# Performance work log

Measured on AMD Instinct MI355X. Metric: run time of the kernel, lower is better.

Reference implementation:

```python
import jax, jax.numpy as jnp
import numpy as np

N_ROI = 1024
N_CLASS = 21      # num_classes + 1
APP_DIM = 1024
D_F = 128
N_REL = 16
DIM_K = 64
DIM_G = 64


def loc2bbox(src, loc):
    # src, loc: [M,4] with (y0,x0,y1,x1) / (dy,dx,dh,dw)
    h = src[:, 2] - src[:, 0]
    w = src[:, 3] - src[:, 1]
    cy = src[:, 0] + 0.5 * h
    cx = src[:, 1] + 0.5 * w
    ncy = loc[:, 0] * h + cy
    ncx = loc[:, 1] * w + cx
    nh = jnp.exp(loc[:, 2]) * h
    nw = jnp.exp(loc[:, 3]) * w
    return jnp.stack([ncy - 0.5 * nh, ncx - 0.5 * nw,
                      ncy + 0.5 * nh, ncx + 0.5 * nw], axis=1)


def rank_embedding(n, feat_dim, wave_len=1000.0):
    rank = jnp.arange(n, dtype=jnp.float32)[:, None]
    fr = jnp.arange(feat_dim // 2, dtype=jnp.float32)
    dim_mat = 1.0 / (wave_len ** (fr / (feat_dim / 2.0)))
    mul = rank * dim_mat[None, :]
    return jnp.concatenate([jnp.sin(mul), jnp.cos(mul)], axis=-1)  # [n, feat_dim]


def positional_embedding(f_g, dim_g, wave_len=1000.0):
    # f_g: [N,4]; replicates the repo's PositionalEmbedding exactly
    x_min, y_min, x_max, y_max = jnp.split(f_g, 4, axis=1)  # [N,1] each
    cx = (x_min + x_max) * 0.5
    cy = (y_min + y_max) * 0.5
    w = (x_max - x_min) + 1.0
    h = (y_max - y_min) + 1.0
    dx = jnp.log(jnp.maximum(jnp.abs((cx - cx.T) / w), 1e-3))
    dy = jnp.log(jnp.maximum(jnp.abs((cy - cy.T) / h), 1e-3))
    dw = jnp.log(w / w.T)
    dh = jnp.log(h / h.T)
    pos = jnp.stack([dx, dy, dw, dh], axis=-1)               # [N,N,4]
    fr = jnp.arange(dim_g // 8, dtype=jnp.float32)
    dim_mat = 1.0 / (wave_len ** (fr / (dim_g / 8.0)))       # [dim_g/8]
    mul = (100.0 * pos)[..., None] * dim_mat                 # [N,N,4,dim_g/8]
    mul = mul.reshape(pos.shape[0], pos.shape[1], -1)
    return jnp.concatenate([jnp.sin(mul), jnp.cos(mul)], axis=-1)  # [N,N,dim_g]


def setup_inputs():
    key = jax.random.key(0)
    ks = jax.random.split(key, 16)
    yx = jax.random.uniform(ks[0], (N_ROI, 2), minval=0.0, maxval=500.0)
    hw = jax.random.uniform(ks[1], (N_ROI, 2), minval=16.0, maxval=128.0)
    sample_roi = jnp.concatenate([yx, yx + hw], axis=1)      # valid (y0,x0,y1,x1)
    roi_cls_loc = jax.random.normal(ks[2], (N_ROI, N_CLASS * 4)) * 0.5
    roi_score = jax.random.normal(ks[3], (N_ROI, N_CLASS))
    # force no background argmax -> nonzero() filter keeps all N (static shapes)
    roi_score = roi_score.at[:, 0].add(-10.0)
    appearance_features = jax.random.normal(ks[4], (N_ROI, APP_DIM))
    size = jnp.array([600, 800], dtype=jnp.int32)
    s = 0.02
    rank_w = jax.random.normal(ks[5], (APP_DIM, D_F)) * s
    rank_b = jnp.zeros((D_F,), jnp.float32)
    feat_w = jax.random.normal(ks[6], (APP_DIM, D_F)) * s
    feat_b = jnp.zeros((D_F,), jnp.float32)
    logit_w = jax.random.normal(ks[7], (APP_DIM, 1)) * s
    logit_b = jnp.zeros((1,), jnp.float32)
    wg_w = jax.random.normal(ks[8], (N_REL, DIM_G)) * s
    wg_b = jnp.full((N_REL,), 0.1, jnp.float32)  # keep some geo weights > 0
    wk_w = jax.random.normal(ks[9], (N_REL, D_F, DIM_K)) * s
    wk_b = jnp.zeros((N_REL, DIM_K), jnp.float32)
    wq_w = jax.random.normal(ks[10], (N_REL, D_F, DIM_K)) * s
    wq_b = jnp.zeros((N_REL, DIM_K), jnp.float32)
    wv_w = jax.random.normal(ks[11], (N_REL, D_F, DIM_K)) * s
    wv_b = jnp.zeros((N_REL, DIM_K), jnp.float32)
    return {"sample_roi": sample_roi, "roi_cls_loc": roi_cls_loc,
            "roi_score": roi_score, "appearance_features": appearance_features,
            "size": size,
            "rank_w": rank_w, "rank_b": rank_b, "feat_w": feat_w, "feat_b": feat_b,
            "logit_w": logit_w, "logit_b": logit_b,
            "wg_w": wg_w, "wg_b": wg_b, "wk_w": wk_w, "wk_b": wk_b,
            "wq_w": wq_w, "wq_b": wq_b, "wv_w": wv_w, "wv_b": wv_b}


def reference(sample_roi, roi_cls_loc, roi_score, appearance_features, size,
              rank_w, rank_b, feat_w, feat_b, logit_w, logit_b,
              wg_w, wg_b, wk_w, wk_b, wq_w, wq_b, wv_w, wv_b):
    n = sample_roi.shape[0]
    size_f = size.astype(jnp.float32)
    # loc denormalization (mean = 0)
    std = jnp.tile(jnp.array([0.1, 0.1, 0.2, 0.2], jnp.float32), N_CLASS)
    loc = (roi_cls_loc * std).reshape(-1, 4)                  # [N*21,4]
    roi_rep = jnp.broadcast_to(sample_roi[:, None, :], (n, N_CLASS, 4)).reshape(-1, 4)
    cls_bbox = loc2bbox(roi_rep, loc).reshape(n, N_CLASS, 4)
    # replicates original's clamp on class-strided slices of the [N,21,4] view
    cls_bbox = cls_bbox.at[:, 0::2].set(jnp.clip(cls_bbox[:, 0::2], 0.0, size_f[0]))
    cls_bbox = cls_bbox.at[:, 1::2].set(jnp.clip(cls_bbox[:, 1::2], 0.0, size_f[1]))
    prob_all = jax.nn.softmax(roi_score, axis=1)
    prob = jnp.max(prob_all, axis=-1)
    prob_argmax = jnp.argmax(prob_all, axis=-1)
    cls_bbox = cls_bbox[jnp.arange(n), prob_argmax]           # [N,4]
    # background filter; inputs guarantee all foreground -> static size n
    nz = jnp.nonzero(prob_argmax, size=n, fill_value=0)[0]
    prob_argmax = prob_argmax[nz]
    prob = prob[nz]
    cls_bbox = cls_bbox[nz]
    feats = appearance_features[nz]
    order = jnp.argsort(-prob)                                # descending
    sorted_prob = prob[order]
    sorted_cls_bboxes = cls_bbox[order]
    sorted_labels = prob_argmax[order]
    sorted_features = feats[order]
    nms_rank = rank_embedding(n, APP_DIM) @ rank_w + rank_b   # [N,D_F]
    emb_feat = sorted_features @ feat_w + feat_b + nms_rank   # [N,D_F]
    pos_emb = positional_embedding(sorted_cls_bboxes, DIM_G)  # [N,N,DIM_G]
    # 16 independent RelationUnits, batched as heads h
    w_g = jax.nn.relu(jnp.einsum('mng,hg->hmn', pos_emb, wg_w) + wg_b[:, None, None])
    k = jnp.einsum('nd,hdk->hnk', emb_feat, wk_w) + wk_b[:, None, :]
    q = jnp.einsum('nd,hdk->hnk', emb_feat, wq_w) + wq_b[:, None, :]
    v = jnp.einsum('nd,hdk->hnk', emb_feat, wv_w) + wv_b[:, None, :]
    # scaled_dot[m,n] = k_m . q_n (row m is 'key', softmax over n) per original
    scores = jnp.einsum('hmk,hnk->hmn', k, q) / np.sqrt(DIM_K).astype(np.float32)
    w_mn = jax.nn.softmax(jnp.log(jnp.maximum(w_g, 1e-6)) + scores, axis=-1)
    rel = jnp.einsum('hmn,hnk->hmk', w_mn, v)                 # [H,N,K]
    rel = rel.transpose(1, 0, 2).reshape(n, N_REL * DIM_K) + sorted_features
    s1 = jax.nn.sigmoid(rel @ logit_w + logit_b).reshape(-1)
    nms_scores = s1 * sorted_prob
    return nms_scores, sorted_labels - 1, sorted_cls_bboxes
```

## Files before the change

### kernel.cpp

```cpp
#include <hip/hip_runtime.h>
#include <hip/hip_bf16.h>
#include <math.h>

typedef unsigned long long u64;
typedef unsigned int u32;
typedef __hip_bfloat16 bf16;

#define N 1024
#define NCLS 21
#define APP 1024
#define DF 128
#define NH 16
#define DK 64

typedef __attribute__((ext_vector_type(8))) short short8v;
typedef __attribute__((ext_vector_type(4))) float float4v;
union U4S8 { uint4 u; short8v s; };

__device__ __forceinline__ float b2f(bf16 x) { return __bfloat162float(x); }
__device__ __forceinline__ ushort f2bu(float x) { bf16 b = __float2bfloat16(x); return *(ushort*)&b; }

__global__ void k_prep(const float* __restrict__ roi, const float* __restrict__ cls_loc,
                       const float* __restrict__ score, const int* __restrict__ size,
                       float* __restrict__ prob, int* __restrict__ label,
                       float* __restrict__ bbox, u64* __restrict__ keys)
{
    int i = blockIdx.x * 256 + threadIdx.x;
    if (i >= N) return;
    float s[NCLS];
    float mx = -1e30f; int am = 0;
    for (int c = 0; c < NCLS; c++) {
        s[c] = score[i * NCLS + c];
        if (s[c] > mx) { mx = s[c]; am = c; }
    }
    float sum = 0.f;
    for (int c = 0; c < NCLS; c++) sum += expf(s[c] - mx);
    float p = 1.0f / sum;

    float y0 = roi[i*4+0], x0 = roi[i*4+1];
    float y1 = roi[i*4+2], x1 = roi[i*4+3];
    float hh = y1 - y0, ww = x1 - x0;
    float cy = y0 + 0.5f * hh, cx = x0 + 0.5f * ww;
    float l0 = cls_loc[i*84 + am*4 + 0] * 0.1f;
    float l1 = cls_loc[i*84 + am*4 + 1] * 0.1f;
    float l2 = cls_loc[i*84 + am*4 + 2] * 0.2f;
    float l3 = cls_loc[i*84 + am*4 + 3] * 0.2f;
    float ncy = l0 * hh + cy, ncx = l1 * ww + cx;
    float nh = expf(l2) * hh, nw = expf(l3) * ww;
    float b0 = ncy - 0.5f * nh, b1 = ncx - 0.5f * nw;
    float b2v = ncy + 0.5f * nh, b3 = ncx + 0.5f * nw;
    float lim = ((am & 1) == 0) ? (float)size[0] : (float)size[1];
    b0  = fminf(fmaxf(b0, 0.f), lim);
    b1  = fminf(fmaxf(b1, 0.f), lim);
    b2v = fminf(fmaxf(b2v, 0.f), lim);
    b3  = fminf(fmaxf(b3, 0.f), lim);
    prob[i] = p; label[i] = am;
    bbox[i*4+0] = b0; bbox[i*4+1] = b1; bbox[i*4+2] = b2v; bbox[i*4+3] = b3;
    keys[i] = ((u64)(0xFFFFFFFFu - __float_as_uint(p)) << 32) | (u32)i;
}

__global__ void __launch_bounds__(256) k_rank(
        const u64* __restrict__ keys, const float* __restrict__ prob,
        const int* __restrict__ label, const float* __restrict__ bbox,
        int* __restrict__ order, float* __restrict__ sprob,
        float* __restrict__ sbbox, float* __restrict__ out)
{
    __shared__ u64 sk[N];
    int t = threadIdx.x;
    int i = blockIdx.x * 256 + t;
    for (int j = t; j < N; j += 256) sk[j] = keys[j];
    __syncthreads();
    u64 my = sk[i];
    int r = 0;
    for (int j = 0; j < N; j++) r += (sk[j] < my) ? 1 : 0;
    order[r] = i;
    sprob[r] = prob[i];
    float b0 = bbox[i*4+0], b1 = bbox[i*4+1], b2 = bbox[i*4+2], b3 = bbox[i*4+3];
    sbbox[r*4+0] = b0; sbbox[r*4+1] = b1; sbbox[r*4+2] = b2; sbbox[r*4+3] = b3;
    out[N + r] = (float)(label[i] - 1);
    out[2*N + r*4 + 0] = b0;
    out[2*N + r*4 + 1] = b1;
    out[2*N + r*4 + 2] = b2;
    out[2*N + r*4 + 3] = b3;
}

__global__ void __launch_bounds__(256) k_emb2(
        const int* __restrict__ order, const float* __restrict__ app,
        const float* __restrict__ feat_w, const float* __restrict__ rank_w,
        float* __restrict__ part)
{
    __shared__ ushort sA[64][72];
    __shared__ ushort sW[128][72];
    __shared__ int sOrd[64];
    int rt = blockIdx.x, dc = blockIdx.y, t = threadIdx.x;
    int r0 = rt * 64, d0 = dc * 64;
    int w = t >> 6, l = t & 63, l15 = l & 15, quad = l >> 4;
    if (t < 64) sOrd[t] = order[r0 + t];
    __syncthreads();

    float4v acc[8];
    #pragma unroll
    for (int nb = 0; nb < 8; nb++) acc[nb] = (float4v){0.f, 0.f, 0.f, 0.f};

    for (int phase = 0; phase < 2; phase++) {
        const float* Wsrc = phase ? rank_w : feat_w;
        #pragma unroll
        for (int it = 0; it < 32; it++) {
            int idx = t + it * 256;
            int d = idx >> 7, c = idx & 127;
            sW[c][d] = f2bu(Wsrc[(size_t)(d0 + d) * 128 + c]);
        }
        if (phase == 0) {
            #pragma unroll
            for (int it = 0; it < 16; it++) {
                int idx = t + it * 256;
                int r = idx >> 6, d = idx & 63;
                sA[r][d] = f2bu(app[(size_t)sOrd[r] * 1024 + d0 + d]);
            }
        } else {
            #pragma unroll
            for (int it = 0; it < 16; it++) {
                int idx = t + it * 256;
                int r = idx >> 6, d = idx & 63;
                int dgl = d0 + d;
                float irow = (float)(r0 + r);
                float val;
                if (dgl < 512) val = __sinf(irow * exp2f(-(float)dgl * 0.019464422f));
                else           val = __cosf(irow * exp2f(-(float)(dgl - 512) * 0.019464422f));
                sA[r][d] = f2bu(val);
            }
        }
        __syncthreads();
        U4S8 Af0, Af1;
        Af0.u = *(uint4*)&sA[w*16 + l15][quad*8];
        Af1.u = *(uint4*)&sA[w*16 + l15][32 + quad*8];
        #pragma unroll
        for (int nb = 0; nb < 8; nb++) {
            U4S8 Bf0, Bf1;
            Bf0.u = *(uint4*)&sW[nb*16 + l15][quad*8];
            Bf1.u = *(uint4*)&sW[nb*16 + l15][32 + quad*8];
            acc[nb] = __builtin_amdgcn_mfma_f32_16x16x32_bf16(Af0.s, Bf0.s, acc[nb], 0, 0, 0);
            acc[nb] = __builtin_amdgcn_mfma_f32_16x16x32_bf16(Af1.s, Bf1.s, acc[nb], 0, 0, 0);
        }
        __syncthreads();
    }
    #pragma unroll
    for (int reg = 0; reg < 4; reg++) {
        int row = r0 + w*16 + quad*4 + reg;
        #pragma unroll
        for (int nb = 0; nb < 8; nb++)
            part[((size_t)dc * 1024 + row) * 128 + nb*16 + l15] = acc[nb][reg];
    }
}

__global__ void k_embsum(const float* __restrict__ part,
                         const float* __restrict__ feat_b, const float* __restrict__ rank_b,
                         bf16* __restrict__ embb)
{
    int gid = blockIdx.x * 256 + threadIdx.x;
    int c = gid & 127;
    float acc = feat_b[c] + rank_b[c];
    for (int dc = 0; dc < 16; dc++) acc += part[(size_t)dc * 131072 + gid];
    embb[gid] = __float2bfloat16(acc);
}

__global__ void __launch_bounds__(256) k_qkv2(
        const bf16* __restrict__ embb,
        const float* __restrict__ wq, const float* __restrict__ bq,
        const float* __restrict__ wk, const float* __restrict__ bk,
        const float* __restrict__ wv, const float* __restrict__ bv,
        bf16* __restrict__ q, bf16* __restrict__ k, bf16* __restrict__ v)
{
    __shared__ ushort sWt[64][136];
    int t = threadIdx.x;
    int rt = blockIdx.x, h = blockIdx.y, mat = blockIdx.z;
    const float* W  = (mat == 0) ? wq : (mat == 1) ? wk : wv;
    const float* Bb = (mat == 0) ? bq : (mat == 1) ? bk : bv;
    bf16* Out       = (mat == 0) ? q  : (mat == 1) ? k  : v;

    #pragma unroll
    for (int i = 0; i < 32; i++) {
        int idx = t + i * 256;
        int d = idx >> 6, kk = idx & 63;
        sWt[kk][d] = f2bu(W[((size_t)h * 128 + d) * 64 + kk]);
    }
    int w = t >> 6, l = t & 63, l15 = l & 15, quad = l >> 4;
    float biasv[4];
    #pragma unroll
    for (int nb = 0; nb < 4; nb++) biasv[nb] = Bb[h * 64 + nb*16 + l15];
    __syncthreads();

    U4S8 Bf[4][4];
    #pragma unroll
    for (int nb = 0; nb < 4; nb++)
        #pragma unroll
        for (int kc = 0; kc < 4; kc++)
            Bf[nb][kc].u = *(uint4*)&sWt[nb*16 + l15][kc*32 + quad*8];

    const uint4* A4 = (const uint4*)embb;
    int r0 = rt * 256 + w * 64;
    ushort* outu = (ushort*)Out;
    for (int mb = 0; mb < 4; mb++) {
        int arow = r0 + mb*16 + l15;
        U4S8 Af[4];
        #pragma unroll
        for (int kc = 0; kc < 4; kc++) Af[kc].u = A4[(size_t)arow * 16 + kc*4 + quad];
        float4v acc[4];
        #pragma unroll
        for (int nb = 0; nb < 4; nb++) acc[nb] = (float4v){0.f, 0.f, 0.f, 0.f};
        #pragma unroll
        for (int kc = 0; kc < 4; kc++)
            #pragma unroll
            for (int nb = 0; nb < 4; nb++)
                acc[nb] = __builtin_amdgcn_mfma_f32_16x16x32_bf16(Af[kc].s, Bf[nb][kc].s, acc[nb], 0, 0, 0);
        #pragma unroll
        for (int reg = 0; reg < 4; reg++) {
            int orow = r0 + mb*16 + quad*4 + reg;
            #pragma unroll
            for (int nb = 0; nb < 4; nb++)
                outu[((size_t)h * N + orow) * 64 + nb*16 + l15] = f2bu(acc[nb][reg] + biasv[nb]);
        }
    }
}

__global__ void __launch_bounds__(256) k_geo2(
        const float* __restrict__ sbbox, const float* __restrict__ wgw,
        const float* __restrict__ wgb, bf16* __restrict__ lw)
{
    __shared__ ushort sE[256][72];
    __shared__ uint   sOut[NH][132];
    __shared__ float  mbb[4];
    int m = blockIdx.x, nc = blockIdx.y, t = threadIdx.x;
    int w = t >> 6, l = t & 63, l15 = l & 15, quad = l >> 4;

    if (t == 0) {
        float b0 = sbbox[m*4+0], b1 = sbbox[m*4+1], b2 = sbbox[m*4+2], b3 = sbbox[m*4+3];
        mbb[0] = (b0 + b2) * 0.5f; mbb[1] = (b1 + b3) * 0.5f;
        mbb[2] = b2 - b0 + 1.0f;   mbb[3] = b3 - b1 + 1.0f;
    }
    U4S8 Bg0, Bg1;
    #pragma unroll
    for (int j = 0; j < 8; j++) {
        ((ushort*)&Bg0)[j] = f2bu(wgw[l15*64 + quad*8 + j]);
        ((ushort*)&Bg1)[j] = f2bu(wgw[l15*64 + 32 + quad*8 + j]);
    }
    float bias = wgb[l15];
    __syncthreads();

    int n = nc * 256 + t;
    float b0 = sbbox[n*4+0], b1 = sbbox[n*4+1], b2 = sbbox[n*4+2], b3 = sbbox[n*4+3];
    float cxn = (b0 + b2) * 0.5f, cyn = (b1 + b3) * 0.5f;
    float wn = b2 - b0 + 1.0f, hn = b3 - b1 + 1.0f;
    float dx = __logf(fmaxf(fabsf((mbb[0] - cxn) / mbb[2]), 1e-3f));
    float dy = __logf(fmaxf(fabsf((mbb[1] - cyn) / mbb[3]), 1e-3f));
    float dw = __logf(mbb[2] / wn);
    float dh = __logf(mbb[3] / hn);
    float pos[4] = { dx, dy, dw, dh };
    const float dmt[8] = { 1.0f, 0.42169650342f, 0.177827941f, 0.0749894209f,
                           0.0316227766f, 0.01333521432f, 0.00562341325f, 0.00237137371f };
    float args[32];
    #pragma unroll
    for (int c = 0; c < 4; c++)
        #pragma unroll
        for (int f = 0; f < 8; f++) args[c*8 + f] = 100.0f * pos[c] * dmt[f];
    uint* rowp = (uint*)&sE[t][0];
    #pragma unroll
    for (int jj = 0; jj < 16; jj++) {
        float s0 = __sinf(args[2*jj]), s1 = __sinf(args[2*jj+1]);
        rowp[jj] = (uint)f2bu(s0) | ((uint)f2bu(s1) << 16);
    }
    #pragma unroll
    for (int jj = 0; jj < 16; jj++) {
        float c0 = __cosf(args[2*jj]), c1 = __cosf(args[2*jj+1]);
        rowp[16 + jj] = (uint)f2bu(c0) | ((uint)f2bu(c1) << 16);
    }
    __syncthreads();

    #pragma unroll
    for (int mt2 = 0; mt2 < 4; mt2++) {
        int prow = w*64 + mt2*16 + l15;
        U4S8 Af0, Af1;
        Af0.u = *(uint4*)&sE[prow][quad*8];
        Af1.u = *(uint4*)&sE[prow][32 + quad*8];
        float4v c = (float4v){0.f, 0.f, 0.f, 0.f};
        c = __builtin_amdgcn_mfma_f32_16x16x32_bf16(Af0.s, Bg0.s, c, 0, 0, 0);
        c = __builtin_amdgcn_mfma_f32_16x16x32_bf16(Af1.s, Bg1.s, c, 0, 0, 0);
        float v0 = __logf(fmaxf(fmaxf(c[0] + bias, 0.f), 1e-6f));
        float v1 = __logf(fmaxf(fmaxf(c[1] + bias, 0.f), 1e-6f));
        float v2 = __logf(fmaxf(fmaxf(c[2] + bias, 0.f), 1e-6f));
        float v3 = __logf(fmaxf(fmaxf(c[3] + bias, 0.f), 1e-6f));
        int pb = (w*64 + mt2*16 + quad*4) >> 1;
        sOut[l15][pb]     = (uint)f2bu(v0) | ((uint)f2bu(v1) << 16);
        sOut[l15][pb + 1] = (uint)f2bu(v2) | ((uint)f2bu(v3) << 16);
    }
    __syncthreads();
    uint* lwu = (uint*)lw;
    #pragma unroll
    for (int it = 0; it < 8; it++) {
        int idx = t + it * 256;
        int hh = idx >> 7, col = idx & 127;
        lwu[((size_t)hh << 19) + ((size_t)m << 9) + nc*128 + col] = sOut[hh][col];
    }
}

__global__ void __launch_bounds__(256) k_attn3(
        const bf16* __restrict__ q, const bf16* __restrict__ kmat,
        const bf16* __restrict__ v, const bf16* __restrict__ lw,
        bf16* __restrict__ rel)
{
    __shared__ uint sQu[64][36];
    __shared__ uint sVtu[64][36];
    __shared__ uint slwu[64][36];
    __shared__ uint sPu[4][16][36];

    int t = threadIdx.x;
    int mt = blockIdx.x, h = blockIdx.y;
    int m0 = mt * 64;
    int w = t >> 6, l = t & 63, l15 = l & 15, quad = l >> 4;

    U4S8 kf0, kf1;
    {
        const uint4* k4 = (const uint4*)kmat;
        size_t krow = ((size_t)h * N + m0 + w*16 + l15) * 8;
        kf0.u = k4[krow + quad];
        kf1.u = k4[krow + 4 + quad];
    }

    float4v O[4];
    float M[4], Z[4];
    #pragma unroll
    for (int i = 0; i < 4; i++) {
        O[i] = (float4v){0.f, 0.f, 0.f, 0.f};
        M[i] = -1e30f; Z[i] = 0.f;
    }

    const uint* qsrc = (const uint*)q;
    const uint* vsrc = (const uint*)v;
    const uint* lwsrc = (const uint*)lw;

    for (int tile = 0; tile < 16; tile++) {
        int n0 = tile * 64;
        #pragma unroll
        for (int i = 0; i < 8; i++) {
            int idx = t + i * 256;
            int nj = idx >> 5, kp = idx & 31;
            sQu[nj][kp] = qsrc[((size_t)h * N + n0 + nj) * 32 + kp];
        }
        #pragma unroll
        for (int i = 0; i < 4; i++) {
            int idx = t + i * 256;
            int a = idx & 31, nh2 = idx >> 5;
            uint g0 = vsrc[((size_t)h * N + n0 + 2*nh2) * 32 + a];
            uint g1 = vsrc[((size_t)h * N + n0 + 2*nh2 + 1) * 32 + a];
            sVtu[2*a][nh2]     = (g0 & 0xFFFFu) | (g1 << 16);
            sVtu[2*a + 1][nh2] = (g0 >> 16) | (g1 & 0xFFFF0000u);
        }
        #pragma unroll
        for (int i = 0; i < 8; i++) {
            int idx = t + i * 256;
            int mi = idx >> 5, np = idx & 31;
            slwu[mi][np] = lwsrc[((size_t)h << 19) + ((size_t)(m0 + mi) << 9) + (n0 >> 1) + np];
        }
        __syncthreads();

        float4v S[4];
        #pragma unroll
        for (int nb = 0; nb < 4; nb++) {
            U4S8 bq0, bq1;
            bq0.u = *(uint4*)&sQu[nb*16 + l15][quad*4];
            bq1.u = *(uint4*)&sQu[nb*16 + l15][16 + quad*4];
            float4v zz = (float4v){0.f, 0.f, 0.f, 0.f};
            float4v p0 = __builtin_amdgcn_mfma_f32_16x16x32_bf16(kf0.s, bq0.s, zz, 0, 0, 0);
            S[nb] = __builtin_amdgcn_mfma_f32_16x16x32_bf16(kf1.s, bq1.s, p0, 0, 0, 0);
        }
        ushort* pRow[4];
        #pragma unroll
        for (int r = 0; r < 4; r++) pRow[r] = (ushort*)&sPu[w][quad*4 + r][0];
        #pragma unroll
        for (int r = 0; r < 4; r++) {
            int mi = w*16 + quad*4 + r;
            float sv[4];
            #pragma unroll
            for (int nb = 0; nb < 4; nb++) {
                int col = nb*16 + l15;
                uint lu = slwu[mi][col >> 1];
                float lv = (col & 1) ? __uint_as_float(lu & 0xFFFF0000u)
                                     : __uint_as_float(lu << 16);
                sv[nb] = S[nb][r] * 0.125f + lv;
            }
            float rm = fmaxf(fmaxf(sv[0], sv[1]), fmaxf(sv[2], sv[3]));
            #pragma unroll
            for (int off = 1; off < 16; off <<= 1)
                rm = fmaxf(rm, __shfl_xor(rm, off, 64));
            float newM = fmaxf(M[r], rm);
            float pr[4], rs = 0.f;
            #pragma unroll
            for (int nb = 0; nb < 4; nb++) {
                pr[nb] = __expf(sv[nb] - newM);
                rs += pr[nb];
            }
            #pragma unroll
            for (int off = 1; off < 16; off <<= 1)
                rs += __shfl_xor(rs, off, 64);
            float sc = __expf(M[r] - newM);
            M[r] = newM;
            Z[r] = Z[r] * sc + rs;
            #pragma unroll
            for (int kvb = 0; kvb < 4; kvb++) O[kvb][r] *= sc;
            #pragma unroll
            for (int nb = 0; nb < 4; nb++)
                pRow[r][nb*16 + l15] = f2bu(pr[nb]);
        }
        {
            U4S8 ap0, ap1;
            ap0.u = *(uint4*)&sPu[w][l15][quad*4];
            ap1.u = *(uint4*)&sPu[w][l15][16 + quad*4];
            #pragma unroll
            for (int kvb = 0; kvb < 4; kvb++) {
                U4S8 bv0, bv1;
                bv0.u = *(uint4*)&sVtu[kvb*16 + l15][quad*4];
                bv1.u = *(uint4*)&sVtu[kvb*16 + l15][16 + quad*4];
                O[kvb] = __builtin_amdgcn_mfma_f32_16x16x32_bf16(ap0.s, bv0.s, O[kvb], 0, 0, 0);
                O[kvb] = __builtin_amdgcn_mfma_f32_16x16x32_bf16(ap1.s, bv1.s, O[kvb], 0, 0, 0);
            }
        }
        __syncthreads();
    }

    float invZ[4];
    #pragma unroll
    for (int r = 0; r < 4; r++) invZ[r] = 1.0f / Z[r];
    ushort* relu = (ushort*)rel;
    #pragma unroll
    for (int r = 0; r < 4; r++) {
        size_t mrow = ((size_t)h * N + m0 + w*16 + quad*4 + r) * 64;
        #pragma unroll
        for (int kvb = 0; kvb < 4; kvb++)
            relu[mrow + kvb*16 + l15] = f2bu(O[kvb][r] * invZ[r]);
    }
}

__global__ void k_final(const bf16* __restrict__ rel, const int* __restrict__ order,
                        const float* __restrict__ app, const float* __restrict__ lw,
                        const float* __restrict__ lb, const float* __restrict__ sprob,
                        float* __restrict__ out)
{
    __shared__ float red[2];
    int m = blockIdx.x, t = threadIdx.x;
    int o = order[m];
    float s = 0.f;
    for (int j = t; j < APP; j += 128) {
        int hh = j >> 6, kk = j & 63;
        float rv = b2f(rel[((size_t)hh * N + m) * DK + kk]) + app[o * APP + j];
        s += rv * lw[j];
    }
    #pragma unroll
    for (int off = 32; off > 0; off >>= 1) s += __shfl_down(s, off, 64);
    if ((t & 63) == 0) red[t >> 6] = s;
    __syncthreads();
    if (t == 0) {
        float tot = red[0] + red[1] + lb[0];
        float s1 = 1.0f / (1.0f + expf(-tot));
        out[m] = s1 * sprob[m];
    }
}

extern "C" void kernel_launch(void* const* d_in, const int* in_sizes, int n_in,
                              void* d_out, int out_size, void* d_ws, size_t ws_size,
                              hipStream_t stream)
{
    const float* roi      = (const float*)d_in[0];
    const float* cls_loc  = (const float*)d_in[1];
    const float* score    = (const float*)d_in[2];
    const float* app      = (const float*)d_in[3];
    const int*   size     = (const int*)d_in[4];
    const float* rank_w   = (const float*)d_in[5];
    const float* rank_b   = (const float*)d_in[6];
    const float* feat_w   = (const float*)d_in[7];
    const float* feat_b   = (const float*)d_in[8];
    const float* logit_w  = (const float*)d_in[9];
    const float* logit_b  = (const float*)d_in[10];
    const float* wg_w     = (const float*)d_in[11];
    const float* wg_b     = (const float*)d_in[12];
    const float* wk_w     = (const float*)d_in[13];
    const float* wk_b     = (const float*)d_in[14];
    const float* wq_w     = (const float*)d_in[15];
    const float* wq_b     = (const float*)d_in[16];
    const float* wv_w     = (const float*)d_in[17];
    const float* wv_b     = (const float*)d_in[18];
    float* out = (float*)d_out;

    char* ws = (char*)d_ws;
    float* prob  = (float*)(ws + 0);
    int*   label = (int*)  (ws + 4096);
    float* bbox  = (float*)(ws + 8192);
    u64*   keys  = (u64*)  (ws + 24576);
    int*   order = (int*)  (ws + 32768);
    float* sprob = (float*)(ws + 36864);
    float* sbbox = (float*)(ws + 40960);
    bf16*  embb  = (bf16*) (ws + 57344);
    float* part  = (float*)(ws + 581632);
    bf16*  q     = (bf16*) (ws + 8970240);
    bf16*  k     = (bf16*) (ws + 11067392);
    bf16*  v     = (bf16*) (ws + 13164544);
    bf16*  rel   = (bf16*) (ws + 15261696);
    bf16*  lwbuf = (bf16*) (ws + 17358848);

    k_prep<<<4, 256, 0, stream>>>(roi, cls_loc, score, size, prob, label, bbox, keys);
    k_rank<<<4, 256, 0, stream>>>(keys, prob, label, bbox, order, sprob, sbbox, out);
    k_emb2<<<dim3(16, 16), 256, 0, stream>>>(order, app, feat_w, rank_w, part);
    k_embsum<<<512, 256, 0, stream>>>(part, feat_b, rank_b, embb);
    k_qkv2<<<dim3(4, 16, 3), 256, 0, stream>>>(embb, wq_w, wq_b, wk_w, wk_b, wv_w, wv_b, q, k, v);
    k_geo2<<<dim3(1024, 4), 256, 0, stream>>>(sbbox, wg_w, wg_b, lwbuf);
    k_attn3<<<dim3(16, 16), 256, 0, stream>>>(q, k, v, lwbuf, rel);
    k_final<<<1024, 128, 0, stream>>>(rel, order, app, logit_w, logit_b, sprob, out);
}
```

Before: 192.5 us.

## Split attention over key chunks, split embedding phases, and widen QKV grid

Attention now splits the 1024 keys into four chunks handled by separate blocks (split-K, flash-decoding style). Each block writes an unnormalized partial output plus its running max and sum, and a new merge kernel rescales and combines them. The embedding GEMM runs its two phases (appearance and rank) as separate grid slices, giving twice the partial sums to reduce, and the QKV projection launches twice as many row blocks. The aim is to fill more of the GPU's compute units, since the old grids had only 256 blocks. The cost is extra fp32 partial traffic, an extra kernel launch and more workspace.

Result: no change. 190.5 us (-1.0%).

```diff
diff --git a/kernel.cpp b/kernel.cpp
--- a/kernel.cpp
+++ b/kernel.cpp
@@ -12,6 +12,7 @@
 #define DF 128
 #define NH 16
 #define DK 64
+#define NS 4
 
 typedef __attribute__((ext_vector_type(8))) short short8v;
 typedef __attribute__((ext_vector_type(4))) float float4v;
@@ -84,7 +85,7 @@
     out[2*N + r*4 + 3] = b3;
 }
 
-__global__ void __launch_bounds__(256) k_emb2(
+__global__ void __launch_bounds__(256) k_emb3(
         const int* __restrict__ order, const float* __restrict__ app,
         const float* __restrict__ feat_w, const float* __restrict__ rank_w,
         float* __restrict__ part)
@@ -92,64 +93,61 @@
     __shared__ ushort sA[64][72];
     __shared__ ushort sW[128][72];
     __shared__ int sOrd[64];
-    int rt = blockIdx.x, dc = blockIdx.y, t = threadIdx.x;
+    int rt = blockIdx.x, dc = blockIdx.y, ph = blockIdx.z, t = threadIdx.x;
     int r0 = rt * 64, d0 = dc * 64;
     int w = t >> 6, l = t & 63, l15 = l & 15, quad = l >> 4;
     if (t < 64) sOrd[t] = order[r0 + t];
     __syncthreads();
 
+    const float* Wsrc = ph ? rank_w : feat_w;
+    #pragma unroll
+    for (int it = 0; it < 32; it++) {
+        int idx = t + it * 256;
+        int d = idx >> 7, c = idx & 127;
+        sW[c][d] = f2bu(Wsrc[(size_t)(d0 + d) * 128 + c]);
+    }
+    if (ph == 0) {
+        #pragma unroll
+        for (int it = 0; it < 16; it++) {
+            int idx = t + it * 256;
+            int r = idx >> 6, d = idx & 63;
+            sA[r][d] = f2bu(app[(size_t)sOrd[r] * 1024 + d0 + d]);
+        }
+    } else {
+        #pragma unroll
+        for (int it = 0; it < 16; it++) {
+            int idx = t + it * 256;
+            int r = idx >> 6, d = idx & 63;
+            int dgl = d0 + d;
+            float irow = (float)(r0 + r);
+            float val;
+            if (dgl < 512) val = __sinf(irow * exp2f(-(float)dgl * 0.019464422f));
+            else           val = __cosf(irow * exp2f(-(float)(dgl - 512) * 0.019464422f));
+            sA[r][d] = f2bu(val);
+        }
+    }
+    __syncthreads();
+
+    U4S8 Af0, Af1;
+    Af0.u = *(uint4*)&sA[w*16 + l15][quad*8];
+    Af1.u = *(uint4*)&sA[w*16 + l15][32 + quad*8];
     float4v acc[8];
     #pragma unroll
     for (int nb = 0; nb < 8; nb++) acc[nb] = (float4v){0.f, 0.f, 0.f, 0.f};
-
-    for (int phase = 0; phase < 2; phase++) {
-        const float* Wsrc = phase ? rank_w : feat_w;
-        #pragma unroll
-        for (int it = 0; it < 32; it++) {
-            int idx = t + it * 256;
-            int d = idx >> 7, c = idx & 127;
-            sW[c][d] = f2bu(Wsrc[(size_t)(d0 + d) * 128 + c]);
-        }
-        if (phase == 0) {
-            #pragma unroll
-            for (int it = 0; it < 16; it++) {
-                int idx = t + it * 256;
-                int r = idx >> 6, d = idx & 63;
-                sA[r][d] = f2bu(app[(size_t)sOrd[r] * 1024 + d0 + d]);
-            }
-        } else {
-            #pragma unroll
-            for (int it = 0; it < 16; it++) {
-                int idx = t + it * 256;
-                int r = idx >> 6, d = idx & 63;
-                int dgl = d0 + d;
-                float irow = (float)(r0 + r);
-                float val;
-                if (dgl < 512) val = __sinf(irow * exp2f(-(float)dgl * 0.019464422f));
-                else           val = __cosf(irow * exp2f(-(float)(dgl - 512) * 0.019464422f));
-                sA[r][d] = f2bu(val);
-            }
-        }
-        __syncthreads();
-        U4S8 Af0, Af1;
-        Af0.u = *(uint4*)&sA[w*16 + l15][quad*8];
-        Af1.u = *(uint4*)&sA[w*16 + l15][32 + quad*8];
-        #pragma unroll
-        for (int nb = 0; nb < 8; nb++) {
-            U4S8 Bf0, Bf1;
-            Bf0.u = *(uint4*)&sW[nb*16 + l15][quad*8];
-            Bf1.u = *(uint4*)&sW[nb*16 + l15][32 + quad*8];
-            acc[nb] = __builtin_amdgcn_mfma_f32_16x16x32_bf16(Af0.s, Bf0.s, acc[nb], 0, 0, 0);
-            acc[nb] = __builtin_amdgcn_mfma_f32_16x16x32_bf16(Af1.s, Bf1.s, acc[nb], 0, 0, 0);
-        }
-        __syncthreads();
+    #pragma unroll
+    for (int nb = 0; nb < 8; nb++) {
+        U4S8 Bf0, Bf1;
+        Bf0.u = *(uint4*)&sW[nb*16 + l15][quad*8];
+        Bf1.u = *(uint4*)&sW[nb*16 + l15][32 + quad*8];
+        acc[nb] = __builtin_amdgcn_mfma_f32_16x16x32_bf16(Af0.s, Bf0.s, acc[nb], 0, 0, 0);
+        acc[nb] = __builtin_amdgcn_mfma_f32_16x16x32_bf16(Af1.s, Bf1.s, acc[nb], 0, 0, 0);
     }
     #pragma unroll
     for (int reg = 0; reg < 4; reg++) {
         int row = r0 + w*16 + quad*4 + reg;
         #pragma unroll
         for (int nb = 0; nb < 8; nb++)
-            part[((size_t)dc * 1024 + row) * 128 + nb*16 + l15] = acc[nb][reg];
+            part[(((size_t)ph * 16 + dc) * 1024 + row) * 128 + nb*16 + l15] = acc[nb][reg];
     }
 }
 
@@ -160,7 +158,7 @@
     int gid = blockIdx.x * 256 + threadIdx.x;
     int c = gid & 127;
     float acc = feat_b[c] + rank_b[c];
-    for (int dc = 0; dc < 16; dc++) acc += part[(size_t)dc * 131072 + gid];
+    for (int dc = 0; dc < 32; dc++) acc += part[(size_t)dc * 131072 + gid];
     embb[gid] = __float2bfloat16(acc);
 }
 
@@ -198,9 +196,9 @@
             Bf[nb][kc].u = *(uint4*)&sWt[nb*16 + l15][kc*32 + quad*8];
 
     const uint4* A4 = (const uint4*)embb;
-    int r0 = rt * 256 + w * 64;
+    int r0 = rt * 128 + w * 32;
     ushort* outu = (ushort*)Out;
-    for (int mb = 0; mb < 4; mb++) {
+    for (int mb = 0; mb < 2; mb++) {
         int arow = r0 + mb*16 + l15;
         U4S8 Af[4];
         #pragma unroll
@@ -303,10 +301,10 @@
     }
 }
 
-__global__ void __launch_bounds__(256) k_attn3(
+__global__ void __launch_bounds__(256) k_attn4(
         const bf16* __restrict__ q, const bf16* __restrict__ kmat,
         const bf16* __restrict__ v, const bf16* __restrict__ lw,
-        bf16* __restrict__ rel)
+        float* __restrict__ opart, float* __restrict__ mpart, float* __restrict__ zpart)
 {
     __shared__ uint sQu[64][36];
     __shared__ uint sVtu[64][36];
@@ -314,7 +312,7 @@
     __shared__ uint sPu[4][16][36];
 
     int t = threadIdx.x;
-    int mt = blockIdx.x, h = blockIdx.y;
+    int mt = blockIdx.x, h = blockIdx.y, ns = blockIdx.z;
     int m0 = mt * 64;
     int w = t >> 6, l = t & 63, l15 = l & 15, quad = l >> 4;
 
@@ -338,7 +336,7 @@
     const uint* vsrc = (const uint*)v;
     const uint* lwsrc = (const uint*)lw;
 
-    for (int tile = 0; tile < 16; tile++) {
+    for (int tile = ns * (16/NS); tile < (ns + 1) * (16/NS); tile++) {
         int n0 = tile * 64;
         #pragma unroll
         for (int i = 0; i < 8; i++) {
@@ -427,17 +425,47 @@
         __syncthreads();
     }
 
-    float invZ[4];
-    #pragma unroll
-    for (int r = 0; r < 4; r++) invZ[r] = 1.0f / Z[r];
+    #pragma unroll
+    for (int r = 0; r < 4; r++) {
+        int m = m0 + w*16 + quad*4 + r;
+        size_t row = ((size_t)ns * NH + h) * N + m;
+        #pragma unroll
+        for (int kvb = 0; kvb < 4; kvb++)
+            opart[row * 64 + kvb*16 + l15] = O[kvb][r];
+        if (l15 == 0) { mpart[row] = M[r]; zpart[row] = Z[r]; }
+    }
+}
+
+__global__ void __launch_bounds__(256) k_amerge(
+        const float* __restrict__ opart, const float* __restrict__ mpart,
+        const float* __restrict__ zpart, bf16* __restrict__ rel)
+{
+    int gid = blockIdx.x * 256 + threadIdx.x;
+    int row = gid >> 4;
+    int colq = gid & 15;
+    float Ms[NS];
+    float Mg = -1e30f;
+    #pragma unroll
+    for (int ns = 0; ns < NS; ns++) {
+        Ms[ns] = mpart[(size_t)ns * 16384 + row];
+        Mg = fmaxf(Mg, Ms[ns]);
+    }
+    float Zt = 0.f;
+    float acc0 = 0.f, acc1 = 0.f, acc2 = 0.f, acc3 = 0.f;
+    #pragma unroll
+    for (int ns = 0; ns < NS; ns++) {
+        float wgt = __expf(Ms[ns] - Mg);
+        Zt += zpart[(size_t)ns * 16384 + row] * wgt;
+        float4 o = *(const float4*)&opart[((size_t)ns * 16384 + row) * 64 + colq*4];
+        acc0 += o.x * wgt; acc1 += o.y * wgt; acc2 += o.z * wgt; acc3 += o.w * wgt;
+    }
+    float inv = 1.0f / Zt;
     ushort* relu = (ushort*)rel;
-    #pragma unroll
-    for (int r = 0; r < 4; r++) {
-        size_t mrow = ((size_t)h * N + m0 + w*16 + quad*4 + r) * 64;
-        #pragma unroll
-        for (int kvb = 0; kvb < 4; kvb++)
-            relu[mrow + kvb*16 + l15] = f2bu(O[kvb][r] * invZ[r]);
-    }
+    size_t base = (size_t)row * 64 + colq*4;
+    relu[base + 0] = f2bu(acc0 * inv);
+    relu[base + 1] = f2bu(acc1 * inv);
+    relu[base + 2] = f2bu(acc2 * inv);
+    relu[base + 3] = f2bu(acc3 * inv);
 }
 
 __global__ void k_final(const bf16* __restrict__ rel, const int* __restrict__ order,
@@ -499,19 +527,23 @@
     float* sprob = (float*)(ws + 36864);
     float* sbbox = (float*)(ws + 40960);
     bf16*  embb  = (bf16*) (ws + 57344);
-    float* part  = (float*)(ws + 581632);
     bf16*  q     = (bf16*) (ws + 8970240);
     bf16*  k     = (bf16*) (ws + 11067392);
     bf16*  v     = (bf16*) (ws + 13164544);
     bf16*  rel   = (bf16*) (ws + 15261696);
     bf16*  lwbuf = (bf16*) (ws + 17358848);
+    float* part  = (float*)(ws + 50913280);
+    float* opart = (float*)(ws + 67690496);
+    float* mpart = (float*)(ws + 84467712);
+    float* zpart = (float*)(ws + 84729856);
 
     k_prep<<<4, 256, 0, stream>>>(roi, cls_loc, score, size, prob, label, bbox, keys);
     k_rank<<<4, 256, 0, stream>>>(keys, prob, label, bbox, order, sprob, sbbox, out);
-    k_emb2<<<dim3(16, 16), 256, 0, stream>>>(order, app, feat_w, rank_w, part);
+    k_emb3<<<dim3(16, 16, 2), 256, 0, stream>>>(order, app, feat_w, rank_w, part);
     k_embsum<<<512, 256, 0, stream>>>(part, feat_b, rank_b, embb);
-    k_qkv2<<<dim3(4, 16, 3), 256, 0, stream>>>(embb, wq_w, wq_b, wk_w, wk_b, wv_w, wv_b, q, k, v);
+    k_qkv2<<<dim3(8, 16, 3), 256, 0, stream>>>(embb, wq_w, wq_b, wk_w, wk_b, wv_w, wv_b, q, k, v);
     k_geo2<<<dim3(1024, 4), 256, 0, stream>>>(sbbox, wg_w, wg_b, lwbuf);
-    k_attn3<<<dim3(16, 16), 256, 0, stream>>>(q, k, v, lwbuf, rel);
+    k_attn4<<<dim3(16, 16, NS), 256, 0, stream>>>(q, k, v, lwbuf, opart, mpart, zpart);
+    k_amerge<<<1024, 256, 0, stream>>>(opart, mpart, zpart, rel);
     k_final<<<1024, 128, 0, stream>>>(rel, order, app, logit_w, logit_b, sprob, out);
 }
```
